# Kernel optimization log

Measured on AMD Instinct MI355X. Metric: run time of the kernel, lower is better.

Reference implementation:

```python
import jax, jax.numpy as jnp
import numpy as np

N = 131072      # number of nodes / samples
IN_DIM = 128    # input_dim
H = 128         # hidden_dim
OUT_DIM = 10    # output_dim


def setup_inputs() -> dict:
    key = jax.random.key(0)
    ks = jax.random.split(key, 20)
    s = 0.05
    def rn(k, shape):
        return jax.random.normal(k, shape, jnp.float32) * s
    return {
        "x": jax.random.normal(ks[0], (N, IN_DIM), jnp.float32),
        # GRU layer 1 (seq_len=1, h0=0 => weight_hh contributes nothing; only b_hh matters)
        "w_ih_f1": rn(ks[1], (3 * H, IN_DIM)), "b_ih_f1": rn(ks[2], (3 * H,)), "b_hh_f1": rn(ks[3], (3 * H,)),
        "w_ih_b1": rn(ks[4], (3 * H, IN_DIM)), "b_ih_b1": rn(ks[5], (3 * H,)), "b_hh_b1": rn(ks[6], (3 * H,)),
        # GRU layer 2 (input 2H)
        "w_ih_f2": rn(ks[7], (3 * H, 2 * H)), "b_ih_f2": rn(ks[8], (3 * H,)), "b_hh_f2": rn(ks[9], (3 * H,)),
        "w_ih_b2": rn(ks[10], (3 * H, 2 * H)), "b_ih_b2": rn(ks[11], (3 * H,)), "b_hh_b2": rn(ks[12], (3 * H,)),
        # GCNConv layers
        "w_g1": rn(ks[13], (2 * H, 128)), "b_g1": rn(ks[14], (128,)),
        "w_g2": rn(ks[15], (128, 64)), "b_g2": rn(ks[16], (64,)),
        # final fc
        "w_fc": rn(ks[17], (64, OUT_DIM)), "b_fc": rn(ks[18], (OUT_DIM,)),
    }


def _gru_cell_zero(x, w_ih, b_ih, b_hh):
    # PyTorch GRU cell with h_prev = 0: h' = (1 - z) * n_gate
    gi = x @ w_ih.T + b_ih                    # [n, 3H]
    ir, iz, inn = jnp.split(gi, 3, axis=-1)
    hr, hz, hn = jnp.split(b_hh, 3)
    r = jax.nn.sigmoid(ir + hr)
    z = jax.nn.sigmoid(iz + hz)
    ng = jnp.tanh(inn + r * hn)
    return (1.0 - z) * ng


def _gcn(x, w, b, sources, targets, n):
    # PyG GCNConv: D^{-1/2}(A+I)D^{-1/2} X W + b, self-loops already in edge lists
    xw = x @ w                                 # [n, out]
    deg = jax.ops.segment_sum(jnp.ones(sources.shape[0], x.dtype), targets, num_segments=n)
    dinv = jax.lax.rsqrt(deg)
    norm = dinv[sources] * dinv[targets]       # [E]
    msg = norm[:, None] * xw[sources]          # gather
    return jax.ops.segment_sum(msg, targets, num_segments=n) + b  # scatter-add


def reference(x, w_ih_f1, b_ih_f1, b_hh_f1, w_ih_b1, b_ih_b1, b_hh_b1,
              w_ih_f2, b_ih_f2, b_hh_f2, w_ih_b2, b_ih_b2, b_hh_b2,
              w_g1, b_g1, w_g2, b_g2, w_fc, b_fc):
    n = x.shape[0]
    # seq_len = 1 => bidirectional GRU output is [fwd_cell(x); bwd_cell(x)]
    h1 = jnp.concatenate([_gru_cell_zero(x, w_ih_f1, b_ih_f1, b_hh_f1),
                          _gru_cell_zero(x, w_ih_b1, b_ih_b1, b_hh_b1)], axis=-1)
    h2 = jnp.concatenate([_gru_cell_zero(h1, w_ih_f2, b_ih_f2, b_hh_f2),
                          _gru_cell_zero(h1, w_ih_b2, b_ih_b2, b_hh_b2)], axis=-1)
    # chain graph, both directions, plus self loops (GCNConv adds them)
    src = jnp.arange(n - 1)
    dst = jnp.arange(1, n)
    ar = jnp.arange(n)
    sources = jnp.concatenate([src, dst, ar])
    targets = jnp.concatenate([dst, src, ar])
    g1 = _gcn(h2, w_g1, b_g1, sources, targets, n)   # dropout is identity in eval
    g2 = _gcn(g1, w_g2, b_g2, sources, targets, n)
    return g2 @ w_fc + b_fc
```

## Files before the change

kernel.cpp:

```cpp
#include <hip/hip_runtime.h>
#include <stdint.h>

#define N_NODES 131072
#define HDIM 128

typedef __bf16 bf16x8 __attribute__((ext_vector_type(8)));
typedef float f32x4 __attribute__((ext_vector_type(4)));
typedef unsigned short us8 __attribute__((ext_vector_type(8)));
typedef unsigned short ushort_t;

__device__ __forceinline__ float bf2f(ushort_t u) {
    union { float f; uint32_t i; } v; v.i = ((uint32_t)u) << 16; return v.f;
}
__device__ __forceinline__ ushort_t f2bf(float f) {
    union { float f; uint32_t i; } v; v.f = f;
    uint32_t i = v.i;
    return (ushort_t)((i + 0x7FFFu + ((i >> 16) & 1u)) >> 16);
}

__device__ __forceinline__ void gll16(const ushort_t* g, ushort_t* l) {
    __builtin_amdgcn_global_load_lds(
        (const __attribute__((address_space(1))) uint32_t*)g,
        (__attribute__((address_space(3))) uint32_t*)l, 16, 0, 0);
}

__device__ __forceinline__ bf16x8 ldsw(const ushort_t* base, int R, int g) {
    return *(const bf16x8*)&base[R * 64 + (((g - R) & 7) << 3)];
}

__device__ __forceinline__ float fsig(float x) {
    return __builtin_amdgcn_rcpf(1.0f + __expf(-x));
}
__device__ __forceinline__ float ftanh(float y) {
    float yc = fminf(fmaxf(y, -15.0f), 15.0f);
    float e = __expf(2.0f * yc);
    return (e - 1.0f) * __builtin_amdgcn_rcpf(e + 1.0f);
}

template<int NC>
__device__ __forceinline__ void swz(int b, int& m, int& c) {
    int mhi = b / (8 * NC);
    int rem = b - mhi * (8 * NC);
    c = rem >> 3;
    m = mhi * 8 + (rem & 7);
}

__global__ __launch_bounds__(256) void prep_all(
    const float* __restrict__ w_f1, const float* __restrict__ w_b1,
    const float* __restrict__ w_f2, const float* __restrict__ w_b2,
    ushort_t* __restrict__ PWF1, ushort_t* __restrict__ PWB1,
    ushort_t* __restrict__ PWF2, ushort_t* __restrict__ PWB2,
    const float* __restrict__ w_g1, const float* __restrict__ b_g1,
    const float* __restrict__ w_g2, const float* __restrict__ b_g2,
    const float* __restrict__ w_fc, const float* __restrict__ b_fc,
    ushort_t* __restrict__ M16, float* __restrict__ cc)
{
    __shared__ float wfc_s[640];
    __shared__ float T1[128][10];
    const int t = threadIdx.x;

    if (blockIdx.x < 1152) {
        int idx = blockIdx.x * 256 + t;
        if (idx < 49152) {
            PWF1[idx] = f2bf(w_f1[idx]);
        } else if (idx < 98304) {
            int j = idx - 49152;  PWB1[j] = f2bf(w_b1[j]);
        } else if (idx < 196608) {
            int j = idx - 98304;  PWF2[j] = f2bf(w_f2[j]);
        } else if (idx < 294912) {
            int j = idx - 196608; PWB2[j] = f2bf(w_b2[j]);
        }
        return;
    }

    for (int i = t; i < 640; i += 256) wfc_s[i] = w_fc[i];
    __syncthreads();
    if (t < 128) {
        float s[10];
        #pragma unroll
        for (int j = 0; j < 10; ++j) s[j] = 0.0f;
        const float4* row = (const float4*)(w_g2 + t * 64);
        #pragma unroll
        for (int k4 = 0; k4 < 16; ++k4) {
            float4 v = row[k4];
            #pragma unroll
            for (int j = 0; j < 10; ++j)
                s[j] += v.x * wfc_s[(k4 * 4 + 0) * 10 + j] + v.y * wfc_s[(k4 * 4 + 1) * 10 + j]
                      + v.z * wfc_s[(k4 * 4 + 2) * 10 + j] + v.w * wfc_s[(k4 * 4 + 3) * 10 + j];
        }
        #pragma unroll
        for (int j = 0; j < 10; ++j) T1[t][j] = s[j];
    }
    __syncthreads();
    float m[10];
    #pragma unroll
    for (int j = 0; j < 10; ++j) m[j] = 0.0f;
    const float4* row1 = (const float4*)(w_g1 + t * 128);
    #pragma unroll 4
    for (int k4 = 0; k4 < 32; ++k4) {
        float4 v = row1[k4];
        #pragma unroll
        for (int j = 0; j < 10; ++j)
            m[j] += v.x * T1[k4 * 4 + 0][j] + v.y * T1[k4 * 4 + 1][j]
                  + v.z * T1[k4 * 4 + 2][j] + v.w * T1[k4 * 4 + 3][j];
    }
    #pragma unroll
    for (int j = 0; j < 16; ++j)
        M16[j * 256 + t] = (j < 10) ? f2bf(m[j]) : (ushort_t)0;
    if (t < 10) {
        float s1 = 0.0f;
        for (int k2 = 0; k2 < 128; ++k2) s1 += b_g1[k2] * T1[k2][t];
        cc[t] = s1;
        float s2 = 0.0f;
        for (int k3 = 0; k3 < 64; ++k3) s2 += b_g2[k3] * wfc_s[k3 * 10 + t];
        cc[16 + t] = s2 + b_fc[t];
    }
}

__global__ __launch_bounds__(256, 5) void gru_l1(
    const float* __restrict__ X,
    const ushort_t* __restrict__ Wf,
    const ushort_t* __restrict__ Wb,
    const float* __restrict__ bi_f, const float* __restrict__ bh_f,
    const float* __restrict__ bi_b, const float* __restrict__ bh_b,
    ushort_t* __restrict__ Hout)
{
    __shared__ ushort_t As[128 * 64];
    __shared__ ushort_t Bs[96 * 64];
    const int tid = threadIdx.x;
    int mt, comb;
    swz<8>(blockIdx.x, mt, comb);
    const int m0 = mt * 128;
    const int dir = comb >> 2;
    const int j0 = (comb & 3) * 32;
    const ushort_t* W = dir ? Wb : Wf;
    const float* b_ih = dir ? bi_b : bi_f;
    const float* b_hh = dir ? bh_b : bh_f;
    const int coloff = dir << 7;

    const int wv = tid >> 6, lane = tid & 63;
    const int lr = lane & 15, lq = lane >> 4;
    const int tr = tid >> 3, tc = tid & 7;
    const int sc = ((tr + tc) & 7) << 3;

    f32x4 acc[3][2][2];
    #pragma unroll
    for (int g = 0; g < 3; ++g)
        #pragma unroll
        for (int rt = 0; rt < 2; ++rt)
            #pragma unroll
            for (int ct = 0; ct < 2; ++ct)
                #pragma unroll
                for (int e = 0; e < 4; ++e) acc[g][rt][ct][e] = 0.0f;

    for (int t = 0; t < 2; ++t) {
        const int k0 = t * 64;
        const float* ga = X + (size_t)(m0 + tr) * 128 + k0 + sc;
        float4 fa[4][2];
        #pragma unroll
        for (int i = 0; i < 4; ++i) {
            const float4* p = (const float4*)(ga + (size_t)i * 32 * 128);
            fa[i][0] = p[0]; fa[i][1] = p[1];
        }
        #pragma unroll
        for (int i = 0; i < 3; ++i) {
            int wr = (i << 7) + j0 + tr;
            gll16(W + (size_t)wr * 128 + k0 + sc, &Bs[(i * 256 + tid) * 8]);
        }
        #pragma unroll
        for (int i = 0; i < 4; ++i) {
            bf16x8 t8;
            t8[0] = (__bf16)fa[i][0].x; t8[1] = (__bf16)fa[i][0].y;
            t8[2] = (__bf16)fa[i][0].z; t8[3] = (__bf16)fa[i][0].w;
            t8[4] = (__bf16)fa[i][1].x; t8[5] = (__bf16)fa[i][1].y;
            t8[6] = (__bf16)fa[i][1].z; t8[7] = (__bf16)fa[i][1].w;
            *(bf16x8*)&As[(i * 256 + tid) * 8] = t8;
        }
        __syncthreads();
        #pragma unroll
        for (int kk = 0; kk < 64; kk += 32) {
            const int g8 = (kk >> 3) + lq;
            bf16x8 a0 = ldsw(As, wv * 32 + lr, g8);
            bf16x8 a1 = ldsw(As, wv * 32 + 16 + lr, g8);
            #pragma unroll
            for (int g = 0; g < 3; ++g) {
                #pragma unroll
                for (int ct = 0; ct < 2; ++ct) {
                    bf16x8 b = ldsw(Bs, g * 32 + ct * 16 + lr, g8);
                    acc[g][0][ct] = __builtin_amdgcn_mfma_f32_16x16x32_bf16(a0, b, acc[g][0][ct], 0, 0, 0);
                    acc[g][1][ct] = __builtin_amdgcn_mfma_f32_16x16x32_bf16(a1, b, acc[g][1][ct], 0, 0, 0);
                }
            }
        }
        __syncthreads();
    }

    #pragma unroll
    for (int ct = 0; ct < 2; ++ct) {
        const int j = j0 + ct * 16 + lr;
        const float br  = b_ih[j] + b_hh[j];
        const float bz  = b_ih[HDIM + j] + b_hh[HDIM + j];
        const float bn  = b_ih[2 * HDIM + j];
        const float bhn = b_hh[2 * HDIM + j];
        #pragma unroll
        for (int rt = 0; rt < 2; ++rt) {
            #pragma unroll
            for (int r = 0; r < 4; ++r) {
                const int row = m0 + wv * 32 + rt * 16 + lq * 4 + r;
                float rg = fsig(acc[0][rt][ct][r] + br);
                float zg = fsig(acc[1][rt][ct][r] + bz);
                float ng = ftanh(acc[2][rt][ct][r] + bn + rg * bhn);
                ((__bf16*)Hout)[(size_t)row * 256 + coloff + j] = (__bf16)((1.0f - zg) * ng);
            }
        }
    }
}

__global__ __launch_bounds__(256, 5) void gru_l2(
    const ushort_t* __restrict__ A,
    const ushort_t* __restrict__ Wf,
    const ushort_t* __restrict__ Wb,
    const float* __restrict__ bi_f, const float* __restrict__ bh_f,
    const float* __restrict__ bi_b, const float* __restrict__ bh_b,
    const ushort_t* __restrict__ M16,
    float* __restrict__ Zp)
{
    __shared__ ushort_t As[128 * 64];
    __shared__ ushort_t Bs[96 * 64];
    const int tid = threadIdx.x;
    int mt, comb;
    swz<8>(blockIdx.x, mt, comb);
    const int m0 = mt * 128;
    const int dir = comb >> 2;
    const int j0 = (comb & 3) * 32;
    const ushort_t* W = dir ? Wb : Wf;
    const float* b_ih = dir ? bi_b : bi_f;
    const float* b_hh = dir ? bh_b : bh_f;
    const int coloff = dir << 7;

    const int wv = tid >> 6, lane = tid & 63;
    const int lr = lane & 15, lq = lane >> 4;
    const int tr = tid >> 3, tc = tid & 7;
    const int sc = ((tr + tc) & 7) << 3;

    f32x4 acc[3][2][2];
    #pragma unroll
    for (int g = 0; g < 3; ++g)
        #pragma unroll
        for (int rt = 0; rt < 2; ++rt)
            #pragma unroll
            for (int ct = 0; ct < 2; ++ct)
                #pragma unroll
                for (int e = 0; e < 4; ++e) acc[g][rt][ct][e] = 0.0f;

    for (int t = 0; t < 4; ++t) {
        const int k0 = t * 64;
        const ushort_t* ga = A + (size_t)(m0 + tr) * 256 + k0 + sc;
        #pragma unroll
        for (int i = 0; i < 4; ++i)
            gll16(ga + (size_t)i * 32 * 256, &As[(i * 256 + tid) * 8]);
        #pragma unroll
        for (int i = 0; i < 3; ++i) {
            int wr = (i << 7) + j0 + tr;
            gll16(W + (size_t)wr * 256 + k0 + sc, &Bs[(i * 256 + tid) * 8]);
        }
        __syncthreads();
        #pragma unroll
        for (int kk = 0; kk < 64; kk += 32) {
            const int g8 = (kk >> 3) + lq;
            bf16x8 a0 = ldsw(As, wv * 32 + lr, g8);
            bf16x8 a1 = ldsw(As, wv * 32 + 16 + lr, g8);
            #pragma unroll
            for (int g = 0; g < 3; ++g) {
                #pragma unroll
                for (int ct = 0; ct < 2; ++ct) {
                    bf16x8 b = ldsw(Bs, g * 32 + ct * 16 + lr, g8);
                    acc[g][0][ct] = __builtin_amdgcn_mfma_f32_16x16x32_bf16(a0, b, acc[g][0][ct], 0, 0, 0);
                    acc[g][1][ct] = __builtin_amdgcn_mfma_f32_16x16x32_bf16(a1, b, acc[g][1][ct], 0, 0, 0);
                }
            }
        }
        __syncthreads();
    }

    const bf16x8 mb = *(const bf16x8*)&M16[lr * 256 + coloff + j0 + lq * 8];

    ushort_t* hs = &As[wv * 1280];
    #pragma unroll
    for (int ct = 0; ct < 2; ++ct) {
        const int j = j0 + ct * 16 + lr;
        const float br  = b_ih[j] + b_hh[j];
        const float bz  = b_ih[HDIM + j] + b_hh[HDIM + j];
        const float bn  = b_ih[2 * HDIM + j];
        const float bhn = b_hh[2 * HDIM + j];
        #pragma unroll
        for (int rt = 0; rt < 2; ++rt) {
            #pragma unroll
            for (int r = 0; r < 4; ++r) {
                const int lrow = rt * 16 + lq * 4 + r;
                float rg = fsig(acc[0][rt][ct][r] + br);
                float zg = fsig(acc[1][rt][ct][r] + bz);
                float ng = ftanh(acc[2][rt][ct][r] + bn + rg * bhn);
                ((__bf16*)hs)[lrow * 40 + ct * 16 + lr] = (__bf16)((1.0f - zg) * ng);
            }
        }
    }
    __syncthreads();

    bf16x8 ha0 = *(const bf16x8*)&hs[lr * 40 + lq * 8];
    bf16x8 ha1 = *(const bf16x8*)&hs[(16 + lr) * 40 + lq * 8];
    f32x4 z0, z1;
    #pragma unroll
    for (int e = 0; e < 4; ++e) { z0[e] = 0.0f; z1[e] = 0.0f; }
    z0 = __builtin_amdgcn_mfma_f32_16x16x32_bf16(ha0, mb, z0, 0, 0, 0);
    z1 = __builtin_amdgcn_mfma_f32_16x16x32_bf16(ha1, mb, z1, 0, 0, 0);

    if (lr < 10) {
        float* zslice = Zp + (size_t)comb * (N_NODES * 10);
        #pragma unroll
        for (int r = 0; r < 4; ++r) {
            zslice[(size_t)(m0 + wv * 32 + lq * 4 + r) * 10 + lr] = z0[r];
            zslice[(size_t)(m0 + wv * 32 + 16 + lq * 4 + r) * 10 + lr] = z1[r];
        }
    }
}

__device__ __forceinline__ float dcoef(int i) {
    return (i == 0 || i == N_NODES - 1) ? 0.70710678118654752f : 0.57735026918962576f;
}
__global__ __launch_bounds__(256) void st5(
    const float* __restrict__ Zp, float* __restrict__ out,
    const float* __restrict__ cc)
{
    int idx = blockIdx.x * 256 + threadIdx.x;
    int i = idx >> 4, c = idx & 15;
    if (c >= 10) return;

    float zk[5];
    #pragma unroll
    for (int o = 0; o < 5; ++o) {
        int k = i + o - 2;
        float v = 0.0f;
        if (k >= 0 && k < N_NODES) {
            #pragma unroll
            for (int s = 0; s < 8; ++s)
                v += Zp[(size_t)s * ((size_t)N_NODES * 10) + (size_t)k * 10 + c];
        }
        zk[o] = v;
    }

    float d_i = dcoef(i);
    float accv = 0.0f, dsum = d_i;
    #pragma unroll
    for (int oj = -1; oj <= 1; ++oj) {
        int j = i + oj;
        if (j < 0 || j >= N_NODES) continue;
        float dj = dcoef(j);
        if (oj != 0) dsum += dj;
        float wj = 0.0f;
        #pragma unroll
        for (int ok = -1; ok <= 1; ++ok) {
            int k = j + ok;
            if (k < 0 || k >= N_NODES) continue;
            wj += dcoef(k) * zk[k - i + 2];
        }
        accv += dj * dj * wj;
    }
    out[(size_t)i * 10 + c] = d_i * accv + d_i * dsum * cc[c] + cc[16 + c];
}

extern "C" void kernel_launch(void* const* d_in, const int* in_sizes, int n_in,
                              void* d_out, int out_size, void* d_ws, size_t ws_size,
                              hipStream_t stream) {
    const float* x     = (const float*)d_in[0];
    const float* w_f1  = (const float*)d_in[1];
    const float* bi_f1 = (const float*)d_in[2];
    const float* bh_f1 = (const float*)d_in[3];
    const float* w_b1  = (const float*)d_in[4];
    const float* bi_b1 = (const float*)d_in[5];
    const float* bh_b1 = (const float*)d_in[6];
    const float* w_f2  = (const float*)d_in[7];
    const float* bi_f2 = (const float*)d_in[8];
    const float* bh_f2 = (const float*)d_in[9];
    const float* w_b2  = (const float*)d_in[10];
    const float* bi_b2 = (const float*)d_in[11];
    const float* bh_b2 = (const float*)d_in[12];
    const float* w_g1  = (const float*)d_in[13];
    const float* b_g1  = (const float*)d_in[14];
    const float* w_g2  = (const float*)d_in[15];
    const float* b_g2  = (const float*)d_in[16];
    const float* w_fc  = (const float*)d_in[17];
    const float* b_fc  = (const float*)d_in[18];

    char* ws = (char*)d_ws;
    ushort_t* h1   = (ushort_t*)(ws);
    float*    Zp   = (float*)(ws + 67108864);
    ushort_t* PWF1 = (ushort_t*)(ws + 134217728);
    ushort_t* PWB1 = PWF1 + 49152;
    ushort_t* PWF2 = PWB1 + 49152;
    ushort_t* PWB2 = PWF2 + 98304;
    ushort_t* M16  = PWB2 + 98304;
    float*    cc   = (float*)(M16 + 4096);

    prep_all<<<1153, 256, 0, stream>>>(w_f1, w_b1, w_f2, w_b2,
                                       PWF1, PWB1, PWF2, PWB2,
                                       w_g1, b_g1, w_g2, b_g2, w_fc, b_fc,
                                       M16, cc);

    gru_l1<<<N_NODES / 128 * 8, 256, 0, stream>>>(
        x, PWF1, PWB1, bi_f1, bh_f1, bi_b1, bh_b1, h1);
    gru_l2<<<N_NODES / 128 * 8, 256, 0, stream>>>(
        h1, PWF2, PWB2, bi_f2, bh_f2, bi_b2, bh_b2, M16, Zp);

    st5<<<N_NODES * 16 / 256, 256, 0, stream>>>(Zp, (float*)d_out, cc);
}
```

Measured before the change: 286.5 us.

## Halve GRU row tiles and split partial-sum reduction out of stencil kernel

Both GRU GEMM kernels now use 64-row tiles instead of 128-row tiles. This doubles the block count, shrinks LDS and accumulator registers per block, and raises the occupancy hint. The cost is that the weight tiles are reloaded twice as often per row. The eight per-column-slice partial results are now summed once by a new vectorised zsum kernel, so the stencil kernel reads one combined array instead of re-summing eight slices for each of its five neighbours. That adds an extra launch and a small intermediate buffer.

```diff
diff --git a/kernel.cpp b/kernel.cpp
--- a/kernel.cpp
+++ b/kernel.cpp
@@ -117,7 +117,7 @@
     }
 }
 
-__global__ __launch_bounds__(256, 5) void gru_l1(
+__global__ __launch_bounds__(256, 7) void gru_l1(
     const float* __restrict__ X,
     const ushort_t* __restrict__ Wf,
     const ushort_t* __restrict__ Wb,
@@ -125,12 +125,12 @@
     const float* __restrict__ bi_b, const float* __restrict__ bh_b,
     ushort_t* __restrict__ Hout)
 {
-    __shared__ ushort_t As[128 * 64];
+    __shared__ ushort_t As[64 * 64];
     __shared__ ushort_t Bs[96 * 64];
     const int tid = threadIdx.x;
     int mt, comb;
     swz<8>(blockIdx.x, mt, comb);
-    const int m0 = mt * 128;
+    const int m0 = mt * 64;
     const int dir = comb >> 2;
     const int j0 = (comb & 3) * 32;
     const ushort_t* W = dir ? Wb : Wf;
@@ -143,32 +143,37 @@
     const int tr = tid >> 3, tc = tid & 7;
     const int sc = ((tr + tc) & 7) << 3;
 
-    f32x4 acc[3][2][2];
+    f32x4 acc[3][2];
     #pragma unroll
     for (int g = 0; g < 3; ++g)
         #pragma unroll
-        for (int rt = 0; rt < 2; ++rt)
+        for (int ct = 0; ct < 2; ++ct)
             #pragma unroll
-            for (int ct = 0; ct < 2; ++ct)
-                #pragma unroll
-                for (int e = 0; e < 4; ++e) acc[g][rt][ct][e] = 0.0f;
+            for (int e = 0; e < 4; ++e) acc[g][ct][e] = 0.0f;
 
     for (int t = 0; t < 2; ++t) {
         const int k0 = t * 64;
         const float* ga = X + (size_t)(m0 + tr) * 128 + k0 + sc;
-        float4 fa[4][2];
-        #pragma unroll
-        for (int i = 0; i < 4; ++i) {
+        float4 fa[2][2];
+        #pragma unroll
+        for (int i = 0; i < 2; ++i) {
             const float4* p = (const float4*)(ga + (size_t)i * 32 * 128);
             fa[i][0] = p[0]; fa[i][1] = p[1];
         }
         #pragma unroll
         for (int i = 0; i < 3; ++i) {
-            int wr = (i << 7) + j0 + tr;
+            int wr = (i << 7) + j0 + ((i * 32 + tr) % 96 == (i * 32 + tr) ? 0 : 0);
+            (void)wr;
+        }
+        #pragma unroll
+        for (int i = 0; i < 3; ++i) {
+            int br_ = i * 32 + tr;
+            int g = br_ >> 5;
+            int wr = (g << 7) + j0 + (br_ & 31);
             gll16(W + (size_t)wr * 128 + k0 + sc, &Bs[(i * 256 + tid) * 8]);
         }
         #pragma unroll
-        for (int i = 0; i < 4; ++i) {
+        for (int i = 0; i < 2; ++i) {
             bf16x8 t8;
             t8[0] = (__bf16)fa[i][0].x; t8[1] = (__bf16)fa[i][0].y;
             t8[2] = (__bf16)fa[i][0].z; t8[3] = (__bf16)fa[i][0].w;
@@ -180,15 +185,13 @@
         #pragma unroll
         for (int kk = 0; kk < 64; kk += 32) {
             const int g8 = (kk >> 3) + lq;
-            bf16x8 a0 = ldsw(As, wv * 32 + lr, g8);
-            bf16x8 a1 = ldsw(As, wv * 32 + 16 + lr, g8);
+            bf16x8 a0 = ldsw(As, wv * 16 + lr, g8);
             #pragma unroll
             for (int g = 0; g < 3; ++g) {
                 #pragma unroll
                 for (int ct = 0; ct < 2; ++ct) {
                     bf16x8 b = ldsw(Bs, g * 32 + ct * 16 + lr, g8);
-                    acc[g][0][ct] = __builtin_amdgcn_mfma_f32_16x16x32_bf16(a0, b, acc[g][0][ct], 0, 0, 0);
-                    acc[g][1][ct] = __builtin_amdgcn_mfma_f32_16x16x32_bf16(a1, b, acc[g][1][ct], 0, 0, 0);
+                    acc[g][ct] = __builtin_amdgcn_mfma_f32_16x16x32_bf16(a0, b, acc[g][ct], 0, 0, 0);
                 }
             }
         }
@@ -203,20 +206,17 @@
         const float bn  = b_ih[2 * HDIM + j];
         const float bhn = b_hh[2 * HDIM + j];
         #pragma unroll
-        for (int rt = 0; rt < 2; ++rt) {
-            #pragma unroll
-            for (int r = 0; r < 4; ++r) {
-                const int row = m0 + wv * 32 + rt * 16 + lq * 4 + r;
-                float rg = fsig(acc[0][rt][ct][r] + br);
-                float zg = fsig(acc[1][rt][ct][r] + bz);
-                float ng = ftanh(acc[2][rt][ct][r] + bn + rg * bhn);
-                ((__bf16*)Hout)[(size_t)row * 256 + coloff + j] = (__bf16)((1.0f - zg) * ng);
-            }
-        }
-    }
-}
-
-__global__ __launch_bounds__(256, 5) void gru_l2(
+        for (int r = 0; r < 4; ++r) {
+            const int row = m0 + wv * 16 + lq * 4 + r;
+            float rg = fsig(acc[0][ct][r] + br);
+            float zg = fsig(acc[1][ct][r] + bz);
+            float ng = ftanh(acc[2][ct][r] + bn + rg * bhn);
+            ((__bf16*)Hout)[(size_t)row * 256 + coloff + j] = (__bf16)((1.0f - zg) * ng);
+        }
+    }
+}
+
+__global__ __launch_bounds__(256, 8) void gru_l2(
     const ushort_t* __restrict__ A,
     const ushort_t* __restrict__ Wf,
     const ushort_t* __restrict__ Wb,
@@ -225,12 +225,12 @@
     const ushort_t* __restrict__ M16,
     float* __restrict__ Zp)
 {
-    __shared__ ushort_t As[128 * 64];
+    __shared__ ushort_t As[64 * 64];
     __shared__ ushort_t Bs[96 * 64];
     const int tid = threadIdx.x;
     int mt, comb;
     swz<8>(blockIdx.x, mt, comb);
-    const int m0 = mt * 128;
+    const int m0 = mt * 64;
     const int dir = comb >> 2;
     const int j0 = (comb & 3) * 32;
     const ushort_t* W = dir ? Wb : Wf;
@@ -243,40 +243,38 @@
     const int tr = tid >> 3, tc = tid & 7;
     const int sc = ((tr + tc) & 7) << 3;
 
-    f32x4 acc[3][2][2];
+    f32x4 acc[3][2];
     #pragma unroll
     for (int g = 0; g < 3; ++g)
         #pragma unroll
-        for (int rt = 0; rt < 2; ++rt)
+        for (int ct = 0; ct < 2; ++ct)
             #pragma unroll
-            for (int ct = 0; ct < 2; ++ct)
-                #pragma unroll
-                for (int e = 0; e < 4; ++e) acc[g][rt][ct][e] = 0.0f;
+            for (int e = 0; e < 4; ++e) acc[g][ct][e] = 0.0f;
 
     for (int t = 0; t < 4; ++t) {
         const int k0 = t * 64;
         const ushort_t* ga = A + (size_t)(m0 + tr) * 256 + k0 + sc;
         #pragma unroll
-        for (int i = 0; i < 4; ++i)
+        for (int i = 0; i < 2; ++i)
             gll16(ga + (size_t)i * 32 * 256, &As[(i * 256 + tid) * 8]);
         #pragma unroll
         for (int i = 0; i < 3; ++i) {
-            int wr = (i << 7) + j0 + tr;
+            int br_ = i * 32 + tr;
+            int g = br_ >> 5;
+            int wr = (g << 7) + j0 + (br_ & 31);
             gll16(W + (size_t)wr * 256 + k0 + sc, &Bs[(i * 256 + tid) * 8]);
         }
         __syncthreads();
         #pragma unroll
         for (int kk = 0; kk < 64; kk += 32) {
             const int g8 = (kk >> 3) + lq;
-            bf16x8 a0 = ldsw(As, wv * 32 + lr, g8);
-            bf16x8 a1 = ldsw(As, wv * 32 + 16 + lr, g8);
+            bf16x8 a0 = ldsw(As, wv * 16 + lr, g8);
             #pragma unroll
             for (int g = 0; g < 3; ++g) {
                 #pragma unroll
                 for (int ct = 0; ct < 2; ++ct) {
                     bf16x8 b = ldsw(Bs, g * 32 + ct * 16 + lr, g8);
-                    acc[g][0][ct] = __builtin_amdgcn_mfma_f32_16x16x32_bf16(a0, b, acc[g][0][ct], 0, 0, 0);
-                    acc[g][1][ct] = __builtin_amdgcn_mfma_f32_16x16x32_bf16(a1, b, acc[g][1][ct], 0, 0, 0);
+                    acc[g][ct] = __builtin_amdgcn_mfma_f32_16x16x32_bf16(a0, b, acc[g][ct], 0, 0, 0);
                 }
             }
         }
@@ -285,7 +283,7 @@
 
     const bf16x8 mb = *(const bf16x8*)&M16[lr * 256 + coloff + j0 + lq * 8];
 
-    ushort_t* hs = &As[wv * 1280];
+    ushort_t* hs = &As[wv * 640];
     #pragma unroll
     for (int ct = 0; ct < 2; ++ct) {
         const int j = j0 + ct * 16 + lr;
@@ -294,61 +292,53 @@
         const float bn  = b_ih[2 * HDIM + j];
         const float bhn = b_hh[2 * HDIM + j];
         #pragma unroll
-        for (int rt = 0; rt < 2; ++rt) {
-            #pragma unroll
-            for (int r = 0; r < 4; ++r) {
-                const int lrow = rt * 16 + lq * 4 + r;
-                float rg = fsig(acc[0][rt][ct][r] + br);
-                float zg = fsig(acc[1][rt][ct][r] + bz);
-                float ng = ftanh(acc[2][rt][ct][r] + bn + rg * bhn);
-                ((__bf16*)hs)[lrow * 40 + ct * 16 + lr] = (__bf16)((1.0f - zg) * ng);
-            }
+        for (int r = 0; r < 4; ++r) {
+            const int lrow = lq * 4 + r;
+            float rg = fsig(acc[0][ct][r] + br);
+            float zg = fsig(acc[1][ct][r] + bz);
+            float ng = ftanh(acc[2][ct][r] + bn + rg * bhn);
+            ((__bf16*)hs)[lrow * 40 + ct * 16 + lr] = (__bf16)((1.0f - zg) * ng);
         }
     }
     __syncthreads();
 
     bf16x8 ha0 = *(const bf16x8*)&hs[lr * 40 + lq * 8];
-    bf16x8 ha1 = *(const bf16x8*)&hs[(16 + lr) * 40 + lq * 8];
-    f32x4 z0, z1;
-    #pragma unroll
-    for (int e = 0; e < 4; ++e) { z0[e] = 0.0f; z1[e] = 0.0f; }
+    f32x4 z0;
+    #pragma unroll
+    for (int e = 0; e < 4; ++e) z0[e] = 0.0f;
     z0 = __builtin_amdgcn_mfma_f32_16x16x32_bf16(ha0, mb, z0, 0, 0, 0);
-    z1 = __builtin_amdgcn_mfma_f32_16x16x32_bf16(ha1, mb, z1, 0, 0, 0);
 
     if (lr < 10) {
-        float* zslice = Zp + (size_t)comb * (N_NODES * 10);
-        #pragma unroll
-        for (int r = 0; r < 4; ++r) {
-            zslice[(size_t)(m0 + wv * 32 + lq * 4 + r) * 10 + lr] = z0[r];
-            zslice[(size_t)(m0 + wv * 32 + 16 + lq * 4 + r) * 10 + lr] = z1[r];
-        }
-    }
+        float* zslice = Zp + (size_t)comb * ((size_t)N_NODES * 10);
+        #pragma unroll
+        for (int r = 0; r < 4; ++r)
+            zslice[(size_t)(m0 + wv * 16 + lq * 4 + r) * 10 + lr] = z0[r];
+    }
+}
+
+__global__ __launch_bounds__(256) void zsum(
+    const float4* __restrict__ Zp4, float4* __restrict__ Zc4)
+{
+    int i = blockIdx.x * 256 + threadIdx.x;
+    float4 a = Zp4[i];
+    #pragma unroll
+    for (int s = 1; s < 8; ++s) {
+        float4 b = Zp4[(size_t)s * 327680 + i];
+        a.x += b.x; a.y += b.y; a.z += b.z; a.w += b.w;
+    }
+    Zc4[i] = a;
 }
 
 __device__ __forceinline__ float dcoef(int i) {
     return (i == 0 || i == N_NODES - 1) ? 0.70710678118654752f : 0.57735026918962576f;
 }
 __global__ __launch_bounds__(256) void st5(
-    const float* __restrict__ Zp, float* __restrict__ out,
+    const float* __restrict__ z, float* __restrict__ out,
     const float* __restrict__ cc)
 {
     int idx = blockIdx.x * 256 + threadIdx.x;
     int i = idx >> 4, c = idx & 15;
     if (c >= 10) return;
-
-    float zk[5];
-    #pragma unroll
-    for (int o = 0; o < 5; ++o) {
-        int k = i + o - 2;
-        float v = 0.0f;
-        if (k >= 0 && k < N_NODES) {
-            #pragma unroll
-            for (int s = 0; s < 8; ++s)
-                v += Zp[(size_t)s * ((size_t)N_NODES * 10) + (size_t)k * 10 + c];
-        }
-        zk[o] = v;
-    }
-
     float d_i = dcoef(i);
     float accv = 0.0f, dsum = d_i;
     #pragma unroll
@@ -362,7 +352,7 @@
         for (int ok = -1; ok <= 1; ++ok) {
             int k = j + ok;
             if (k < 0 || k >= N_NODES) continue;
-            wj += dcoef(k) * zk[k - i + 2];
+            wj += dcoef(k) * z[(size_t)k * 10 + c];
         }
         accv += dj * dj * wj;
     }
@@ -395,6 +385,7 @@
     char* ws = (char*)d_ws;
     ushort_t* h1   = (ushort_t*)(ws);
     float*    Zp   = (float*)(ws + 67108864);
+    float*    Zc   = (float*)(ws + 109051904);
     ushort_t* PWF1 = (ushort_t*)(ws + 134217728);
     ushort_t* PWB1 = PWF1 + 49152;
     ushort_t* PWF2 = PWB1 + 49152;
@@ -407,10 +398,11 @@
                                        w_g1, b_g1, w_g2, b_g2, w_fc, b_fc,
                                        M16, cc);
 
-    gru_l1<<<N_NODES / 128 * 8, 256, 0, stream>>>(
+    gru_l1<<<N_NODES / 64 * 8, 256, 0, stream>>>(
         x, PWF1, PWB1, bi_f1, bh_f1, bi_b1, bh_b1, h1);
-    gru_l2<<<N_NODES / 128 * 8, 256, 0, stream>>>(
+    gru_l2<<<N_NODES / 64 * 8, 256, 0, stream>>>(
         h1, PWF2, PWB2, bi_f2, bh_f2, bi_b2, bh_b2, M16, Zp);
 
-    st5<<<N_NODES * 16 / 256, 256, 0, stream>>>(Zp, (float*)d_out, cc);
-}
+    zsum<<<1280, 256, 0, stream>>>((const float4*)Zp, (float4*)Zc);
+    st5<<<N_NODES * 16 / 256, 256, 0, stream>>>(Zc, (float*)d_out, cc);
+}
```

Measured after the change: 311.5 us. 8.7% more time.

## Widen GRU column tiles to 64 and pre-reduce partial Z slices

Applied to the files above, without the earlier changes.

Both GRU kernels now compute 64 hidden columns per block instead of 32, halving the grid and the number of times each row tile of X/h1 is loaded, with larger LDS for the weights and more accumulators. The layer-2 epilogue projects the wider tile with two MFMAs, so there are 4 partial Z slices instead of 8. A new zsum kernel sums those slices once, so the stencil kernel reads a single Z array rather than re-summing 8 slices for each of its 5 neighbors. This trades occupancy (launch bounds drop from 5 to 3) and an extra kernel launch for less redundant global traffic.

```diff
diff --git a/kernel.cpp b/kernel.cpp
--- a/kernel.cpp
+++ b/kernel.cpp
@@ -117,7 +117,7 @@
     }
 }
 
-__global__ __launch_bounds__(256, 5) void gru_l1(
+__global__ __launch_bounds__(256, 3) void gru_l1(
     const float* __restrict__ X,
     const ushort_t* __restrict__ Wf,
     const ushort_t* __restrict__ Wb,
@@ -126,13 +126,13 @@
     ushort_t* __restrict__ Hout)
 {
     __shared__ ushort_t As[128 * 64];
-    __shared__ ushort_t Bs[96 * 64];
+    __shared__ ushort_t Bs[192 * 64];
     const int tid = threadIdx.x;
     int mt, comb;
-    swz<8>(blockIdx.x, mt, comb);
+    swz<4>(blockIdx.x, mt, comb);
     const int m0 = mt * 128;
-    const int dir = comb >> 2;
-    const int j0 = (comb & 3) * 32;
+    const int dir = comb >> 1;
+    const int j0 = (comb & 1) * 64;
     const ushort_t* W = dir ? Wb : Wf;
     const float* b_ih = dir ? bi_b : bi_f;
     const float* b_hh = dir ? bh_b : bh_f;
@@ -143,13 +143,13 @@
     const int tr = tid >> 3, tc = tid & 7;
     const int sc = ((tr + tc) & 7) << 3;
 
-    f32x4 acc[3][2][2];
+    f32x4 acc[3][2][4];
     #pragma unroll
     for (int g = 0; g < 3; ++g)
         #pragma unroll
         for (int rt = 0; rt < 2; ++rt)
             #pragma unroll
-            for (int ct = 0; ct < 2; ++ct)
+            for (int ct = 0; ct < 4; ++ct)
                 #pragma unroll
                 for (int e = 0; e < 4; ++e) acc[g][rt][ct][e] = 0.0f;
 
@@ -163,8 +163,9 @@
             fa[i][0] = p[0]; fa[i][1] = p[1];
         }
         #pragma unroll
-        for (int i = 0; i < 3; ++i) {
-            int wr = (i << 7) + j0 + tr;
+        for (int i = 0; i < 6; ++i) {
+            int rb = i * 32 + tr;
+            int wr = (rb >> 6) * 128 + j0 + (rb & 63);
             gll16(W + (size_t)wr * 128 + k0 + sc, &Bs[(i * 256 + tid) * 8]);
         }
         #pragma unroll
@@ -185,8 +186,8 @@
             #pragma unroll
             for (int g = 0; g < 3; ++g) {
                 #pragma unroll
-                for (int ct = 0; ct < 2; ++ct) {
-                    bf16x8 b = ldsw(Bs, g * 32 + ct * 16 + lr, g8);
+                for (int ct = 0; ct < 4; ++ct) {
+                    bf16x8 b = ldsw(Bs, g * 64 + ct * 16 + lr, g8);
                     acc[g][0][ct] = __builtin_amdgcn_mfma_f32_16x16x32_bf16(a0, b, acc[g][0][ct], 0, 0, 0);
                     acc[g][1][ct] = __builtin_amdgcn_mfma_f32_16x16x32_bf16(a1, b, acc[g][1][ct], 0, 0, 0);
                 }
@@ -196,7 +197,7 @@
     }
 
     #pragma unroll
-    for (int ct = 0; ct < 2; ++ct) {
+    for (int ct = 0; ct < 4; ++ct) {
         const int j = j0 + ct * 16 + lr;
         const float br  = b_ih[j] + b_hh[j];
         const float bz  = b_ih[HDIM + j] + b_hh[HDIM + j];
@@ -216,7 +217,7 @@
     }
 }
 
-__global__ __launch_bounds__(256, 5) void gru_l2(
+__global__ __launch_bounds__(256, 3) void gru_l2(
     const ushort_t* __restrict__ A,
     const ushort_t* __restrict__ Wf,
     const ushort_t* __restrict__ Wb,
@@ -226,30 +227,29 @@
     float* __restrict__ Zp)
 {
     __shared__ ushort_t As[128 * 64];
-    __shared__ ushort_t Bs[96 * 64];
+    __shared__ ushort_t Bs[192 * 64];
     const int tid = threadIdx.x;
     int mt, comb;
-    swz<8>(blockIdx.x, mt, comb);
+    swz<4>(blockIdx.x, mt, comb);
     const int m0 = mt * 128;
-    const int dir = comb >> 2;
-    const int j0 = (comb & 3) * 32;
+    const int dir = comb >> 1;
+    const int j0 = (comb & 1) * 64;
     const ushort_t* W = dir ? Wb : Wf;
     const float* b_ih = dir ? bi_b : bi_f;
     const float* b_hh = dir ? bh_b : bh_f;
-    const int coloff = dir << 7;
 
     const int wv = tid >> 6, lane = tid & 63;
     const int lr = lane & 15, lq = lane >> 4;
     const int tr = tid >> 3, tc = tid & 7;
     const int sc = ((tr + tc) & 7) << 3;
 
-    f32x4 acc[3][2][2];
+    f32x4 acc[3][2][4];
     #pragma unroll
     for (int g = 0; g < 3; ++g)
         #pragma unroll
         for (int rt = 0; rt < 2; ++rt)
             #pragma unroll
-            for (int ct = 0; ct < 2; ++ct)
+            for (int ct = 0; ct < 4; ++ct)
                 #pragma unroll
                 for (int e = 0; e < 4; ++e) acc[g][rt][ct][e] = 0.0f;
 
@@ -260,8 +260,9 @@
         for (int i = 0; i < 4; ++i)
             gll16(ga + (size_t)i * 32 * 256, &As[(i * 256 + tid) * 8]);
         #pragma unroll
-        for (int i = 0; i < 3; ++i) {
-            int wr = (i << 7) + j0 + tr;
+        for (int i = 0; i < 6; ++i) {
+            int rb = i * 32 + tr;
+            int wr = (rb >> 6) * 128 + j0 + (rb & 63);
             gll16(W + (size_t)wr * 256 + k0 + sc, &Bs[(i * 256 + tid) * 8]);
         }
         __syncthreads();
@@ -273,8 +274,8 @@
             #pragma unroll
             for (int g = 0; g < 3; ++g) {
                 #pragma unroll
-                for (int ct = 0; ct < 2; ++ct) {
-                    bf16x8 b = ldsw(Bs, g * 32 + ct * 16 + lr, g8);
+                for (int ct = 0; ct < 4; ++ct) {
+                    bf16x8 b = ldsw(Bs, g * 64 + ct * 16 + lr, g8);
                     acc[g][0][ct] = __builtin_amdgcn_mfma_f32_16x16x32_bf16(a0, b, acc[g][0][ct], 0, 0, 0);
                     acc[g][1][ct] = __builtin_amdgcn_mfma_f32_16x16x32_bf16(a1, b, acc[g][1][ct], 0, 0, 0);
                 }
@@ -283,16 +284,19 @@
         __syncthreads();
     }
 
-    const bf16x8 mb = *(const bf16x8*)&M16[lr * 256 + coloff + j0 + lq * 8];
-
-    ushort_t* hs = &As[wv * 1280];
-    #pragma unroll
-    for (int ct = 0; ct < 2; ++ct) {
+    const bf16x8 mb0 = *(const bf16x8*)&M16[lr * 256 + (dir << 7) + j0 + lq * 8];
+    const bf16x8 mb1 = *(const bf16x8*)&M16[lr * 256 + (dir << 7) + j0 + 32 + lq * 8];
+
+    ushort_t* hs = &Bs[wv * 2560];
+    #pragma unroll
+    for (int ct = 0; ct < 4; ++ct) {
         const int j = j0 + ct * 16 + lr;
         const float br  = b_ih[j] + b_hh[j];
         const float bz  = b_ih[HDIM + j] + b_hh[HDIM + j];
         const float bn  = b_ih[2 * HDIM + j];
         const float bhn = b_hh[2 * HDIM + j];
+        const int kc = ct >> 1;
+        const int lcol = (ct & 1) * 16 + lr;
         #pragma unroll
         for (int rt = 0; rt < 2; ++rt) {
             #pragma unroll
@@ -301,54 +305,58 @@
                 float rg = fsig(acc[0][rt][ct][r] + br);
                 float zg = fsig(acc[1][rt][ct][r] + bz);
                 float ng = ftanh(acc[2][rt][ct][r] + bn + rg * bhn);
-                ((__bf16*)hs)[lrow * 40 + ct * 16 + lr] = (__bf16)((1.0f - zg) * ng);
+                ((__bf16*)hs)[kc * 1280 + lrow * 40 + lcol] = (__bf16)((1.0f - zg) * ng);
             }
         }
     }
     __syncthreads();
 
-    bf16x8 ha0 = *(const bf16x8*)&hs[lr * 40 + lq * 8];
-    bf16x8 ha1 = *(const bf16x8*)&hs[(16 + lr) * 40 + lq * 8];
-    f32x4 z0, z1;
-    #pragma unroll
-    for (int e = 0; e < 4; ++e) { z0[e] = 0.0f; z1[e] = 0.0f; }
-    z0 = __builtin_amdgcn_mfma_f32_16x16x32_bf16(ha0, mb, z0, 0, 0, 0);
-    z1 = __builtin_amdgcn_mfma_f32_16x16x32_bf16(ha1, mb, z1, 0, 0, 0);
+    f32x4 z[2];
+    #pragma unroll
+    for (int rt = 0; rt < 2; ++rt)
+        #pragma unroll
+        for (int e = 0; e < 4; ++e) z[rt][e] = 0.0f;
+    #pragma unroll
+    for (int rt = 0; rt < 2; ++rt) {
+        bf16x8 ha0 = *(const bf16x8*)&hs[(rt * 16 + lr) * 40 + lq * 8];
+        bf16x8 ha1 = *(const bf16x8*)&hs[1280 + (rt * 16 + lr) * 40 + lq * 8];
+        z[rt] = __builtin_amdgcn_mfma_f32_16x16x32_bf16(ha0, mb0, z[rt], 0, 0, 0);
+        z[rt] = __builtin_amdgcn_mfma_f32_16x16x32_bf16(ha1, mb1, z[rt], 0, 0, 0);
+    }
 
     if (lr < 10) {
-        float* zslice = Zp + (size_t)comb * (N_NODES * 10);
-        #pragma unroll
-        for (int r = 0; r < 4; ++r) {
-            zslice[(size_t)(m0 + wv * 32 + lq * 4 + r) * 10 + lr] = z0[r];
-            zslice[(size_t)(m0 + wv * 32 + 16 + lq * 4 + r) * 10 + lr] = z1[r];
-        }
-    }
+        float* zslice = Zp + (size_t)comb * ((size_t)N_NODES * 10);
+        #pragma unroll
+        for (int rt = 0; rt < 2; ++rt)
+            #pragma unroll
+            for (int r = 0; r < 4; ++r)
+                zslice[(size_t)(m0 + wv * 32 + rt * 16 + lq * 4 + r) * 10 + lr] = z[rt][r];
+    }
+}
+
+__global__ __launch_bounds__(256) void zsum(
+    const float4* __restrict__ Zp4, float4* __restrict__ Zc4)
+{
+    int i = blockIdx.x * 256 + threadIdx.x;
+    float4 a = Zp4[i];
+    #pragma unroll
+    for (int s = 1; s < 4; ++s) {
+        float4 b = Zp4[(size_t)s * 327680 + i];
+        a.x += b.x; a.y += b.y; a.z += b.z; a.w += b.w;
+    }
+    Zc4[i] = a;
 }
 
 __device__ __forceinline__ float dcoef(int i) {
     return (i == 0 || i == N_NODES - 1) ? 0.70710678118654752f : 0.57735026918962576f;
 }
 __global__ __launch_bounds__(256) void st5(
-    const float* __restrict__ Zp, float* __restrict__ out,
+    const float* __restrict__ z, float* __restrict__ out,
     const float* __restrict__ cc)
 {
     int idx = blockIdx.x * 256 + threadIdx.x;
     int i = idx >> 4, c = idx & 15;
     if (c >= 10) return;
-
-    float zk[5];
-    #pragma unroll
-    for (int o = 0; o < 5; ++o) {
-        int k = i + o - 2;
-        float v = 0.0f;
-        if (k >= 0 && k < N_NODES) {
-            #pragma unroll
-            for (int s = 0; s < 8; ++s)
-                v += Zp[(size_t)s * ((size_t)N_NODES * 10) + (size_t)k * 10 + c];
-        }
-        zk[o] = v;
-    }
-
     float d_i = dcoef(i);
     float accv = 0.0f, dsum = d_i;
     #pragma unroll
@@ -362,7 +370,7 @@
         for (int ok = -1; ok <= 1; ++ok) {
             int k = j + ok;
             if (k < 0 || k >= N_NODES) continue;
-            wj += dcoef(k) * zk[k - i + 2];
+            wj += dcoef(k) * z[(size_t)k * 10 + c];
         }
         accv += dj * dj * wj;
     }
@@ -395,6 +403,7 @@
     char* ws = (char*)d_ws;
     ushort_t* h1   = (ushort_t*)(ws);
     float*    Zp   = (float*)(ws + 67108864);
+    float*    Zc   = (float*)(ws + 109051904);
     ushort_t* PWF1 = (ushort_t*)(ws + 134217728);
     ushort_t* PWB1 = PWF1 + 49152;
     ushort_t* PWF2 = PWB1 + 49152;
@@ -407,10 +416,11 @@
                                        w_g1, b_g1, w_g2, b_g2, w_fc, b_fc,
                                        M16, cc);
 
-    gru_l1<<<N_NODES / 128 * 8, 256, 0, stream>>>(
+    gru_l1<<<N_NODES / 128 * 4, 256, 0, stream>>>(
         x, PWF1, PWB1, bi_f1, bh_f1, bi_b1, bh_b1, h1);
-    gru_l2<<<N_NODES / 128 * 8, 256, 0, stream>>>(
+    gru_l2<<<N_NODES / 128 * 4, 256, 0, stream>>>(
         h1, PWF2, PWB2, bi_f2, bh_f2, bi_b2, bh_b2, M16, Zp);
 
-    st5<<<N_NODES * 16 / 256, 256, 0, stream>>>(Zp, (float*)d_out, cc);
-}
+    zsum<<<1280, 256, 0, stream>>>((const float4*)Zp, (float4*)Zc);
+    st5<<<N_NODES * 16 / 256, 256, 0, stream>>>(Zc, (float*)d_out, cc);
+}
```

Result: slower. 297.0 us (+3.7%).

## Double-buffer GRU GEMM K-loop and tile stencil kernel through shared memory

Applied to the files above, without the earlier changes.

Both GRU kernels now use a 32-wide K slice with two LDS buffers, so the global/LDS loads for the next slice are issued before the MFMAs on the current one and one barrier per iteration is dropped. The LDS swizzle is adapted to 32-column rows and occupancy hint drops from 5 to 4 on layer 1. The final stencil kernel now stages the 8-way summed Z partials for 260 nodes in shared memory once per block instead of each thread re-reading 5 neighbours from 8 slices, cutting redundant global reads roughly fivefold. Smaller K slices mean more iterations and barriers, which may offset the overlap gains.

```diff
diff --git a/kernel.cpp b/kernel.cpp
--- a/kernel.cpp
+++ b/kernel.cpp
@@ -9,9 +9,6 @@
 typedef unsigned short us8 __attribute__((ext_vector_type(8)));
 typedef unsigned short ushort_t;
 
-__device__ __forceinline__ float bf2f(ushort_t u) {
-    union { float f; uint32_t i; } v; v.i = ((uint32_t)u) << 16; return v.f;
-}
 __device__ __forceinline__ ushort_t f2bf(float f) {
     union { float f; uint32_t i; } v; v.f = f;
     uint32_t i = v.i;
@@ -24,8 +21,8 @@
         (__attribute__((address_space(3))) uint32_t*)l, 16, 0, 0);
 }
 
-__device__ __forceinline__ bf16x8 ldsw(const ushort_t* base, int R, int g) {
-    return *(const bf16x8*)&base[R * 64 + (((g - R) & 7) << 3)];
+__device__ __forceinline__ bf16x8 ldsw32(const ushort_t* base, int R, int g) {
+    return *(const bf16x8*)&base[R * 32 + (((g - (R >> 1)) & 3) << 3)];
 }
 
 __device__ __forceinline__ float fsig(float x) {
@@ -117,7 +114,7 @@
     }
 }
 
-__global__ __launch_bounds__(256, 5) void gru_l1(
+__global__ __launch_bounds__(256, 4) void gru_l1(
     const float* __restrict__ X,
     const ushort_t* __restrict__ Wf,
     const ushort_t* __restrict__ Wb,
@@ -125,8 +122,8 @@
     const float* __restrict__ bi_b, const float* __restrict__ bh_b,
     ushort_t* __restrict__ Hout)
 {
-    __shared__ ushort_t As[128 * 64];
-    __shared__ ushort_t Bs[96 * 64];
+    __shared__ ushort_t As[2][128 * 32];
+    __shared__ ushort_t Bs[2][96 * 32];
     const int tid = threadIdx.x;
     int mt, comb;
     swz<8>(blockIdx.x, mt, comb);
@@ -140,8 +137,22 @@
 
     const int wv = tid >> 6, lane = tid & 63;
     const int lr = lane & 15, lq = lane >> 4;
-    const int tr = tid >> 3, tc = tid & 7;
-    const int sc = ((tr + tc) & 7) << 3;
+
+    int arow[2], agk[2];
+    #pragma unroll
+    for (int p = 0; p < 2; ++p) {
+        int ci = p * 256 + tid;
+        arow[p] = ci >> 2;
+        agk[p] = (((ci & 3) + (arow[p] >> 1)) & 3) << 3;
+    }
+    int bwr[2], bgk[2];
+    #pragma unroll
+    for (int p = 0; p < 2; ++p) {
+        int ci = p * 256 + tid;
+        int rb = ci >> 2;
+        bgk[p] = (((ci & 3) + (rb >> 1)) & 3) << 3;
+        bwr[p] = ((rb >> 5) << 7) + j0 + (rb & 31);
+    }
 
     f32x4 acc[3][2][2];
     #pragma unroll
@@ -153,46 +164,67 @@
                 #pragma unroll
                 for (int e = 0; e < 4; ++e) acc[g][rt][ct][e] = 0.0f;
 
-    for (int t = 0; t < 2; ++t) {
-        const int k0 = t * 64;
-        const float* ga = X + (size_t)(m0 + tr) * 128 + k0 + sc;
-        float4 fa[4][2];
-        #pragma unroll
-        for (int i = 0; i < 4; ++i) {
-            const float4* p = (const float4*)(ga + (size_t)i * 32 * 128);
-            fa[i][0] = p[0]; fa[i][1] = p[1];
-        }
-        #pragma unroll
-        for (int i = 0; i < 3; ++i) {
-            int wr = (i << 7) + j0 + tr;
-            gll16(W + (size_t)wr * 128 + k0 + sc, &Bs[(i * 256 + tid) * 8]);
-        }
-        #pragma unroll
-        for (int i = 0; i < 4; ++i) {
-            bf16x8 t8;
-            t8[0] = (__bf16)fa[i][0].x; t8[1] = (__bf16)fa[i][0].y;
-            t8[2] = (__bf16)fa[i][0].z; t8[3] = (__bf16)fa[i][0].w;
-            t8[4] = (__bf16)fa[i][1].x; t8[5] = (__bf16)fa[i][1].y;
-            t8[6] = (__bf16)fa[i][1].z; t8[7] = (__bf16)fa[i][1].w;
-            *(bf16x8*)&As[(i * 256 + tid) * 8] = t8;
-        }
+    float4 xa[2][2];
+    #pragma unroll
+    for (int p = 0; p < 2; ++p) {
+        const float4* src = (const float4*)(X + (size_t)(m0 + arow[p]) * 128 + agk[p]);
+        xa[p][0] = src[0]; xa[p][1] = src[1];
+    }
+    gll16(W + (size_t)bwr[0] * 128 + bgk[0], &Bs[0][tid * 8]);
+    if (tid < 128)
+        gll16(W + (size_t)bwr[1] * 128 + bgk[1], &Bs[0][(256 + tid) * 8]);
+    #pragma unroll
+    for (int p = 0; p < 2; ++p) {
+        bf16x8 t8;
+        t8[0] = (__bf16)xa[p][0].x; t8[1] = (__bf16)xa[p][0].y;
+        t8[2] = (__bf16)xa[p][0].z; t8[3] = (__bf16)xa[p][0].w;
+        t8[4] = (__bf16)xa[p][1].x; t8[5] = (__bf16)xa[p][1].y;
+        t8[6] = (__bf16)xa[p][1].z; t8[7] = (__bf16)xa[p][1].w;
+        *(bf16x8*)&As[0][(p * 256 + tid) * 8] = t8;
+    }
+
+    int cur = 0;
+    for (int t = 0; t < 4; ++t) {
         __syncthreads();
-        #pragma unroll
-        for (int kk = 0; kk < 64; kk += 32) {
-            const int g8 = (kk >> 3) + lq;
-            bf16x8 a0 = ldsw(As, wv * 32 + lr, g8);
-            bf16x8 a1 = ldsw(As, wv * 32 + 16 + lr, g8);
+        const int nxt = cur ^ 1;
+        if (t + 1 < 4) {
+            const int k0n = (t + 1) * 32;
+            #pragma unroll
+            for (int p = 0; p < 2; ++p) {
+                const float4* src = (const float4*)(X + (size_t)(m0 + arow[p]) * 128 + k0n + agk[p]);
+                xa[p][0] = src[0]; xa[p][1] = src[1];
+            }
+            gll16(W + (size_t)bwr[0] * 128 + k0n + bgk[0], &Bs[nxt][tid * 8]);
+            if (tid < 128)
+                gll16(W + (size_t)bwr[1] * 128 + k0n + bgk[1], &Bs[nxt][(256 + tid) * 8]);
+        }
+        {
+            const ushort_t* Ac = &As[cur][0];
+            const ushort_t* Bc = &Bs[cur][0];
+            bf16x8 a0 = ldsw32(Ac, wv * 32 + lr, lq);
+            bf16x8 a1 = ldsw32(Ac, wv * 32 + 16 + lr, lq);
             #pragma unroll
             for (int g = 0; g < 3; ++g) {
                 #pragma unroll
                 for (int ct = 0; ct < 2; ++ct) {
-                    bf16x8 b = ldsw(Bs, g * 32 + ct * 16 + lr, g8);
+                    bf16x8 b = ldsw32(Bc, g * 32 + ct * 16 + lr, lq);
                     acc[g][0][ct] = __builtin_amdgcn_mfma_f32_16x16x32_bf16(a0, b, acc[g][0][ct], 0, 0, 0);
                     acc[g][1][ct] = __builtin_amdgcn_mfma_f32_16x16x32_bf16(a1, b, acc[g][1][ct], 0, 0, 0);
                 }
             }
         }
-        __syncthreads();
+        if (t + 1 < 4) {
+            #pragma unroll
+            for (int p = 0; p < 2; ++p) {
+                bf16x8 t8;
+                t8[0] = (__bf16)xa[p][0].x; t8[1] = (__bf16)xa[p][0].y;
+                t8[2] = (__bf16)xa[p][0].z; t8[3] = (__bf16)xa[p][0].w;
+                t8[4] = (__bf16)xa[p][1].x; t8[5] = (__bf16)xa[p][1].y;
+                t8[6] = (__bf16)xa[p][1].z; t8[7] = (__bf16)xa[p][1].w;
+                *(bf16x8*)&As[nxt][(p * 256 + tid) * 8] = t8;
+            }
+        }
+        cur = nxt;
     }
 
     #pragma unroll
@@ -225,8 +257,8 @@
     const ushort_t* __restrict__ M16,
     float* __restrict__ Zp)
 {
-    __shared__ ushort_t As[128 * 64];
-    __shared__ ushort_t Bs[96 * 64];
+    __shared__ ushort_t As[2][128 * 32];
+    __shared__ ushort_t Bs[2][96 * 32];
     const int tid = threadIdx.x;
     int mt, comb;
     swz<8>(blockIdx.x, mt, comb);
@@ -240,8 +272,22 @@
 
     const int wv = tid >> 6, lane = tid & 63;
     const int lr = lane & 15, lq = lane >> 4;
-    const int tr = tid >> 3, tc = tid & 7;
-    const int sc = ((tr + tc) & 7) << 3;
+
+    int arow[2], agk[2];
+    #pragma unroll
+    for (int p = 0; p < 2; ++p) {
+        int ci = p * 256 + tid;
+        arow[p] = ci >> 2;
+        agk[p] = (((ci & 3) + (arow[p] >> 1)) & 3) << 3;
+    }
+    int bwr[2], bgk[2];
+    #pragma unroll
+    for (int p = 0; p < 2; ++p) {
+        int ci = p * 256 + tid;
+        int rb = ci >> 2;
+        bgk[p] = (((ci & 3) + (rb >> 1)) & 3) << 3;
+        bwr[p] = ((rb >> 5) << 7) + j0 + (rb & 31);
+    }
 
     f32x4 acc[3][2][2];
     #pragma unroll
@@ -253,39 +299,49 @@
                 #pragma unroll
                 for (int e = 0; e < 4; ++e) acc[g][rt][ct][e] = 0.0f;
 
-    for (int t = 0; t < 4; ++t) {
-        const int k0 = t * 64;
-        const ushort_t* ga = A + (size_t)(m0 + tr) * 256 + k0 + sc;
-        #pragma unroll
-        for (int i = 0; i < 4; ++i)
-            gll16(ga + (size_t)i * 32 * 256, &As[(i * 256 + tid) * 8]);
-        #pragma unroll
-        for (int i = 0; i < 3; ++i) {
-            int wr = (i << 7) + j0 + tr;
-            gll16(W + (size_t)wr * 256 + k0 + sc, &Bs[(i * 256 + tid) * 8]);
-        }
+    #pragma unroll
+    for (int p = 0; p < 2; ++p)
+        gll16(A + (size_t)(m0 + arow[p]) * 256 + agk[p], &As[0][(p * 256 + tid) * 8]);
+    gll16(W + (size_t)bwr[0] * 256 + bgk[0], &Bs[0][tid * 8]);
+    if (tid < 128)
+        gll16(W + (size_t)bwr[1] * 256 + bgk[1], &Bs[0][(256 + tid) * 8]);
+
+    int cur = 0;
+    for (int t = 0; t < 8; ++t) {
         __syncthreads();
-        #pragma unroll
-        for (int kk = 0; kk < 64; kk += 32) {
-            const int g8 = (kk >> 3) + lq;
-            bf16x8 a0 = ldsw(As, wv * 32 + lr, g8);
-            bf16x8 a1 = ldsw(As, wv * 32 + 16 + lr, g8);
+        const int nxt = cur ^ 1;
+        if (t + 1 < 8) {
+            const int k0n = (t + 1) * 32;
+            #pragma unroll
+            for (int p = 0; p < 2; ++p)
+                gll16(A + (size_t)(m0 + arow[p]) * 256 + k0n + agk[p],
+                      &As[nxt][(p * 256 + tid) * 8]);
+            gll16(W + (size_t)bwr[0] * 256 + k0n + bgk[0], &Bs[nxt][tid * 8]);
+            if (tid < 128)
+                gll16(W + (size_t)bwr[1] * 256 + k0n + bgk[1], &Bs[nxt][(256 + tid) * 8]);
+        }
+        {
+            const ushort_t* Ac = &As[cur][0];
+            const ushort_t* Bc = &Bs[cur][0];
+            bf16x8 a0 = ldsw32(Ac, wv * 32 + lr, lq);
+            bf16x8 a1 = ldsw32(Ac, wv * 32 + 16 + lr, lq);
             #pragma unroll
             for (int g = 0; g < 3; ++g) {
                 #pragma unroll
                 for (int ct = 0; ct < 2; ++ct) {
-                    bf16x8 b = ldsw(Bs, g * 32 + ct * 16 + lr, g8);
+                    bf16x8 b = ldsw32(Bc, g * 32 + ct * 16 + lr, lq);
                     acc[g][0][ct] = __builtin_amdgcn_mfma_f32_16x16x32_bf16(a0, b, acc[g][0][ct], 0, 0, 0);
                     acc[g][1][ct] = __builtin_amdgcn_mfma_f32_16x16x32_bf16(a1, b, acc[g][1][ct], 0, 0, 0);
                 }
             }
         }
-        __syncthreads();
-    }
+        cur = nxt;
+    }
+    __syncthreads();
 
     const bf16x8 mb = *(const bf16x8*)&M16[lr * 256 + coloff + j0 + lq * 8];
 
-    ushort_t* hs = &As[wv * 1280];
+    ushort_t* hs = &As[0][0] + wv * 1280;
     #pragma unroll
     for (int ct = 0; ct < 2; ++ct) {
         const int j = j0 + ct * 16 + lr;
@@ -316,7 +372,7 @@
     z1 = __builtin_amdgcn_mfma_f32_16x16x32_bf16(ha1, mb, z1, 0, 0, 0);
 
     if (lr < 10) {
-        float* zslice = Zp + (size_t)comb * (N_NODES * 10);
+        float* zslice = Zp + (size_t)comb * ((size_t)N_NODES * 10);
         #pragma unroll
         for (int r = 0; r < 4; ++r) {
             zslice[(size_t)(m0 + wv * 32 + lq * 4 + r) * 10 + lr] = z0[r];
@@ -328,45 +384,53 @@
 __device__ __forceinline__ float dcoef(int i) {
     return (i == 0 || i == N_NODES - 1) ? 0.70710678118654752f : 0.57735026918962576f;
 }
-__global__ __launch_bounds__(256) void st5(
+__global__ __launch_bounds__(256) void stz(
     const float* __restrict__ Zp, float* __restrict__ out,
     const float* __restrict__ cc)
 {
-    int idx = blockIdx.x * 256 + threadIdx.x;
-    int i = idx >> 4, c = idx & 15;
-    if (c >= 10) return;
-
-    float zk[5];
-    #pragma unroll
-    for (int o = 0; o < 5; ++o) {
-        int k = i + o - 2;
+    __shared__ float zl[260 * 10];
+    const int tid = threadIdx.x;
+    const int n0 = blockIdx.x * 256;
+
+    for (int i = tid; i < 2600; i += 256) {
+        int nl = i / 10;
+        int c = i - nl * 10;
+        int n = n0 - 2 + nl;
         float v = 0.0f;
-        if (k >= 0 && k < N_NODES) {
+        if (n >= 0 && n < N_NODES) {
+            size_t base = (size_t)n * 10 + c;
             #pragma unroll
             for (int s = 0; s < 8; ++s)
-                v += Zp[(size_t)s * ((size_t)N_NODES * 10) + (size_t)k * 10 + c];
-        }
-        zk[o] = v;
-    }
-
-    float d_i = dcoef(i);
-    float accv = 0.0f, dsum = d_i;
-    #pragma unroll
-    for (int oj = -1; oj <= 1; ++oj) {
-        int j = i + oj;
-        if (j < 0 || j >= N_NODES) continue;
-        float dj = dcoef(j);
-        if (oj != 0) dsum += dj;
-        float wj = 0.0f;
-        #pragma unroll
-        for (int ok = -1; ok <= 1; ++ok) {
-            int k = j + ok;
-            if (k < 0 || k >= N_NODES) continue;
-            wj += dcoef(k) * zk[k - i + 2];
-        }
-        accv += dj * dj * wj;
-    }
-    out[(size_t)i * 10 + c] = d_i * accv + d_i * dsum * cc[c] + cc[16 + c];
+                v += Zp[(size_t)s * ((size_t)N_NODES * 10) + base];
+        }
+        zl[i] = v;
+    }
+    __syncthreads();
+
+    const int i = n0 + tid;
+    const float d_i = dcoef(i);
+    float dsum = d_i;
+    if (i - 1 >= 0) dsum += dcoef(i - 1);
+    if (i + 1 < N_NODES) dsum += dcoef(i + 1);
+
+    #pragma unroll
+    for (int c = 0; c < 10; ++c) {
+        float accv = 0.0f;
+        #pragma unroll
+        for (int oj = -1; oj <= 1; ++oj) {
+            int j = i + oj;
+            if (j < 0 || j >= N_NODES) continue;
+            float dj = dcoef(j);
+            float wj = 0.0f;
+            #pragma unroll
+            for (int ok = -1; ok <= 1; ++ok) {
+                int k = j + ok;
+                wj += dcoef(k) * zl[(tid + 2 + oj + ok) * 10 + c];
+            }
+            accv += dj * dj * wj;
+        }
+        out[(size_t)i * 10 + c] = d_i * accv + d_i * dsum * cc[c] + cc[16 + c];
+    }
 }
 
 extern "C" void kernel_launch(void* const* d_in, const int* in_sizes, int n_in,
@@ -412,5 +476,5 @@
     gru_l2<<<N_NODES / 128 * 8, 256, 0, stream>>>(
         h1, PWF2, PWB2, bi_f2, bh_f2, bi_b2, bh_b2, M16, Zp);
 
-    st5<<<N_NODES * 16 / 256, 256, 0, stream>>>(Zp, (float*)d_out, cc);
-}
+    stz<<<N_NODES / 256, 256, 0, stream>>>(Zp, (float*)d_out, cc);
+}
```

Result: slower. 308.3 us (+7.6%).
